# Kernel tuning notes

Measured on AMD Instinct MI355X. Metric: run time of the kernel, lower is better.

Reference implementation:

```python
import jax, jax.numpy as jnp
import numpy as np


def setup_inputs() -> dict:
    key = jax.random.key(0)
    kq, kk, kv = jax.random.split(key, 3)
    B, H, N, D = 4, 16, 2048, 64
    q = jax.random.normal(kq, (B, H, N, D), dtype=jnp.float32)
    k = jax.random.normal(kk, (B, N, D), dtype=jnp.float32)
    v = jax.random.normal(kv, (B, N, D), dtype=jnp.float32)
    return {"q": q, "k": k, "v": v}


def reference(q, k, v):
    # q: [B,H,N,D], k/v: [B,N,D] (KV shared across heads)
    scale = q.shape[-1] ** -0.5
    sim = jnp.einsum('bhid,bjd->bhij', q, k) * scale  # [B,H,N,N]
    attn = jax.nn.softmax(sim, axis=-1)
    return jnp.einsum('bhij,bjd->bhid', attn, v)  # [B,H,N,D]
```

## Files before the change

kernel.cpp:

```cpp
#include <hip/hip_runtime.h>
#include <hip/hip_bf16.h>

#define B_ 4
#define H_ 16
#define N_ 2048
#define D_ 64
#define BM 128

typedef __bf16 bf16;
typedef bf16 bf16x4 __attribute__((ext_vector_type(4)));
typedef bf16 bf16x8 __attribute__((ext_vector_type(8)));
typedef float f32x16 __attribute__((ext_vector_type(16)));
typedef unsigned u32x2 __attribute__((ext_vector_type(2)));
typedef unsigned u32x4 __attribute__((ext_vector_type(4)));

#define SCALE_LOG2E 0.18033688011112042f

#define GBL(p) ((const __attribute__((address_space(1))) void*)(p))
#define LDS(p) ((__attribute__((address_space(3))) void*)(p))

__global__ __launch_bounds__(512) void convert_kv(const float* __restrict__ k,
                                                  const float* __restrict__ v,
                                                  bf16* __restrict__ img) {
    __shared__ bf16 VT[64][66];
    const int tile = blockIdx.x;
    const int b = tile >> 5, T = tile & 31;
    const int t = threadIdx.x;
    bf16* timg = img + (size_t)tile * 8192;

    const int mtks = t >> 6;
    const int ln   = t & 63;
    const int mt = mtks >> 2, ks = mtks & 3;

    {
        const int kvr = T * 64 + mt * 32 + (ln & 31);
        const int d0  = ks * 16 + (ln >> 5) * 8;
        const float* src = k + ((size_t)b * N_ + kvr) * D_ + d0;
        float4 a = *(const float4*)src;
        float4 c = *(const float4*)(src + 4);
        bf16x8 o;
        o[0] = (bf16)a.x; o[1] = (bf16)a.y; o[2] = (bf16)a.z; o[3] = (bf16)a.w;
        o[4] = (bf16)c.x; o[5] = (bf16)c.y; o[6] = (bf16)c.z; o[7] = (bf16)c.w;
        *(bf16x8*)(timg + t * 8) = o;
    }

    {
        const int kv = t >> 3;
        const int c8 = (t & 7) * 8;
        const float* src = v + ((size_t)b * N_ + T * 64 + kv) * D_ + c8;
        float4 a = *(const float4*)src;
        float4 c = *(const float4*)(src + 4);
        VT[kv][c8 + 0] = (bf16)a.x; VT[kv][c8 + 1] = (bf16)a.y;
        VT[kv][c8 + 2] = (bf16)a.z; VT[kv][c8 + 3] = (bf16)a.w;
        VT[kv][c8 + 4] = (bf16)c.x; VT[kv][c8 + 5] = (bf16)c.y;
        VT[kv][c8 + 6] = (bf16)c.z; VT[kv][c8 + 7] = (bf16)c.w;
    }
    __syncthreads();
    {
        const int d   = mt * 32 + (ln & 31);
        const int kv0 = ks * 16 + (ln >> 5) * 8;
        bf16x8 o;
        #pragma unroll
        for (int j = 0; j < 8; ++j) o[j] = VT[kv0 + j][d];
        *(bf16x8*)(timg + 4096 + t * 8) = o;
    }
}

static __device__ inline bf16x4 pack4(float a, float b, float c, float d) {
    bf16x4 r; r[0] = (bf16)a; r[1] = (bf16)b; r[2] = (bf16)c; r[3] = (bf16)d; return r;
}

static __device__ inline bf16x8 cswap(bf16x4 lo, bf16x4 hi) {
    u32x2 l = __builtin_bit_cast(u32x2, lo);
    u32x2 h = __builtin_bit_cast(u32x2, hi);
    u32x2 r0 = __builtin_amdgcn_permlane32_swap(l[0], h[0], false, false);
    u32x2 r1 = __builtin_amdgcn_permlane32_swap(l[1], h[1], false, false);
    u32x4 o; o[0] = r0[0]; o[1] = r1[0]; o[2] = r0[1]; o[3] = r1[1];
    return __builtin_bit_cast(bf16x8, o);
}

__global__ __launch_bounds__(256, 2) void attn_fwd(const float* __restrict__ q,
                                                   const bf16* __restrict__ img,
                                                   float* __restrict__ out) {
    __shared__ __align__(16) bf16 KV3[3][8192];

    const int tid  = threadIdx.x;
    const int lane = tid & 63;
    const int wv   = tid >> 6;
    const int half = lane >> 5;
    const int l31  = lane & 31;

    const int bh = blockIdx.y;
    const int b  = bh >> 4;
    const int q0 = blockIdx.x * BM + wv * 32;

    const bf16* tiles = img + (size_t)b * 32 * 8192;

    bf16x8 qf[4];
    #pragma unroll
    for (int ks = 0; ks < 4; ++ks) {
        const float* src = q + ((size_t)bh * N_ + q0 + l31) * D_ + ks * 16 + half * 8;
        float4 a = *(const float4*)src;
        float4 c = *(const float4*)(src + 4);
        bf16x8 pk;
        pk[0] = (bf16)(a.x * SCALE_LOG2E); pk[1] = (bf16)(a.y * SCALE_LOG2E);
        pk[2] = (bf16)(a.z * SCALE_LOG2E); pk[3] = (bf16)(a.w * SCALE_LOG2E);
        pk[4] = (bf16)(c.x * SCALE_LOG2E); pk[5] = (bf16)(c.y * SCALE_LOG2E);
        pk[6] = (bf16)(c.z * SCALE_LOG2E); pk[7] = (bf16)(c.w * SCALE_LOG2E);
        qf[ks] = pk;
    }

    f32x16 acc[2] = {{}, {}};
    float lacc = 0.f;

    auto issue_dma = [&](int t, int sl) {
        const bf16* g = tiles + (size_t)t * 8192;
        #pragma unroll
        for (int j = 0; j < 4; ++j) {
            const int c = wv * 4 + j;
            __builtin_amdgcn_global_load_lds(GBL(g + c * 512 + lane * 8),
                                             LDS(&KV3[sl][c * 512]), 16, 0, 0);
        }
    };

    auto computeS = [&](int it, f32x16 (&s)[2]) {
        const bf16* bp = &KV3[it % 3][0];
        s[0] = f32x16{}; s[1] = f32x16{};
        #pragma unroll
        for (int ks = 0; ks < 4; ++ks) {
            bf16x8 k0 = *(const bf16x8*)&bp[((0 * 4 + ks) * 64 + lane) * 8];
            bf16x8 k1 = *(const bf16x8*)&bp[((1 * 4 + ks) * 64 + lane) * 8];
            s[0] = __builtin_amdgcn_mfma_f32_32x32x16_bf16(k0, qf[ks], s[0], 0, 0, 0);
            s[1] = __builtin_amdgcn_mfma_f32_32x32x16_bf16(k1, qf[ks], s[1], 0, 0, 0);
        }
    };
    auto softpv = [&](int it, const f32x16 (&s)[2]) {
        const bf16* vp = &KV3[it % 3][4096];
        #pragma unroll
        for (int mt = 0; mt < 2; ++mt) {
            #pragma unroll
            for (int sp = 0; sp < 2; ++sp) {
                const int g = mt * 2 + sp;
                bf16x8 v0 = *(const bf16x8*)&vp[((0 * 4 + g) * 64 + lane) * 8];
                bf16x8 v1 = *(const bf16x8*)&vp[((1 * 4 + g) * 64 + lane) * 8];
                float pv8[8];
                #pragma unroll
                for (int r = 0; r < 8; ++r) pv8[r] = __builtin_amdgcn_exp2f(s[mt][8 * sp + r]);
                lacc += ((pv8[0] + pv8[1]) + (pv8[2] + pv8[3]))
                      + ((pv8[4] + pv8[5]) + (pv8[6] + pv8[7]));
                bf16x4 lo = pack4(pv8[0], pv8[1], pv8[2], pv8[3]);
                bf16x4 hi = pack4(pv8[4], pv8[5], pv8[6], pv8[7]);
                bf16x8 bfrag = cswap(lo, hi);
                acc[0] = __builtin_amdgcn_mfma_f32_32x32x16_bf16(v0, bfrag, acc[0], 0, 0, 0);
                acc[1] = __builtin_amdgcn_mfma_f32_32x32x16_bf16(v1, bfrag, acc[1], 0, 0, 0);
            }
        }
    };

    f32x16 sA[2], sB[2];

    issue_dma(0, 0);
    __syncthreads();
    issue_dma(1, 1);
    computeS(0, sA);

    #pragma unroll 1
    for (int it = 1; it < 31; it += 2) {
        __syncthreads();
        issue_dma(it + 1, (it + 1) % 3);
        computeS(it, sB);
        softpv(it - 1, sA);
        __syncthreads();
        issue_dma(it + 2, (it + 2) % 3);
        computeS(it + 1, sA);
        softpv(it, sB);
    }
    __syncthreads();
    computeS(31, sB);
    softpv(30, sA);
    softpv(31, sB);

    float l = lacc + __shfl_xor(lacc, 32);
    float inv = 1.0f / l;
    const int qrow = q0 + l31;
    float* dst = out + ((size_t)bh * N_ + qrow) * D_ + 4 * half;
    #pragma unroll
    for (int mt = 0; mt < 2; ++mt)
        #pragma unroll
        for (int rq = 0; rq < 4; ++rq) {
            float4 o;
            o.x = acc[mt][4 * rq + 0] * inv;
            o.y = acc[mt][4 * rq + 1] * inv;
            o.z = acc[mt][4 * rq + 2] * inv;
            o.w = acc[mt][4 * rq + 3] * inv;
            *(float4*)(dst + mt * 32 + 8 * rq) = o;
        }
}

extern "C" void kernel_launch(void* const* d_in, const int* in_sizes, int n_in,
                              void* d_out, int out_size, void* d_ws, size_t ws_size,
                              hipStream_t stream) {
    const float* q = (const float*)d_in[0];
    const float* k = (const float*)d_in[1];
    const float* v = (const float*)d_in[2];
    float* out = (float*)d_out;

    bf16* img = (bf16*)d_ws;

    convert_kv<<<B_ * 32, 512, 0, stream>>>(k, v, img);
    dim3 grid(N_ / BM, B_ * H_);
    attn_fwd<<<grid, 256, 0, stream>>>(q, img, out);
}
```

Baseline: 152.5 us.

## Split S tiles into halves to cut registers and raise occupancy to three blocks

Result: slower. 156.8 us (+2.8%).

```diff
diff --git a/kernel.cpp b/kernel.cpp
--- a/kernel.cpp
+++ b/kernel.cpp
@@ -79,7 +79,7 @@
     return __builtin_bit_cast(bf16x8, o);
 }
 
-__global__ __launch_bounds__(256, 2) void attn_fwd(const float* __restrict__ q,
+__global__ __launch_bounds__(256, 3) void attn_fwd(const float* __restrict__ q,
                                                    const bf16* __restrict__ img,
                                                    float* __restrict__ out) {
     __shared__ __align__(16) bf16 KV3[3][8192];
@@ -123,62 +123,51 @@
         }
     };
 
-    auto computeS = [&](int it, f32x16 (&s)[2]) {
+    auto computeS_h = [&](int it, int mt, f32x16 &s) {
         const bf16* bp = &KV3[it % 3][0];
-        s[0] = f32x16{}; s[1] = f32x16{};
+        s = f32x16{};
         #pragma unroll
         for (int ks = 0; ks < 4; ++ks) {
-            bf16x8 k0 = *(const bf16x8*)&bp[((0 * 4 + ks) * 64 + lane) * 8];
-            bf16x8 k1 = *(const bf16x8*)&bp[((1 * 4 + ks) * 64 + lane) * 8];
-            s[0] = __builtin_amdgcn_mfma_f32_32x32x16_bf16(k0, qf[ks], s[0], 0, 0, 0);
-            s[1] = __builtin_amdgcn_mfma_f32_32x32x16_bf16(k1, qf[ks], s[1], 0, 0, 0);
+            bf16x8 kf = *(const bf16x8*)&bp[((mt * 4 + ks) * 64 + lane) * 8];
+            s = __builtin_amdgcn_mfma_f32_32x32x16_bf16(kf, qf[ks], s, 0, 0, 0);
         }
     };
-    auto softpv = [&](int it, const f32x16 (&s)[2]) {
+    auto softpv_h = [&](int it, int mt, const f32x16 &s) {
         const bf16* vp = &KV3[it % 3][4096];
         #pragma unroll
-        for (int mt = 0; mt < 2; ++mt) {
+        for (int sp = 0; sp < 2; ++sp) {
+            const int g = mt * 2 + sp;
+            bf16x8 v0 = *(const bf16x8*)&vp[((0 * 4 + g) * 64 + lane) * 8];
+            bf16x8 v1 = *(const bf16x8*)&vp[((1 * 4 + g) * 64 + lane) * 8];
+            float pv8[8];
             #pragma unroll
-            for (int sp = 0; sp < 2; ++sp) {
-                const int g = mt * 2 + sp;
-                bf16x8 v0 = *(const bf16x8*)&vp[((0 * 4 + g) * 64 + lane) * 8];
-                bf16x8 v1 = *(const bf16x8*)&vp[((1 * 4 + g) * 64 + lane) * 8];
-                float pv8[8];
-                #pragma unroll
-                for (int r = 0; r < 8; ++r) pv8[r] = __builtin_amdgcn_exp2f(s[mt][8 * sp + r]);
-                lacc += ((pv8[0] + pv8[1]) + (pv8[2] + pv8[3]))
-                      + ((pv8[4] + pv8[5]) + (pv8[6] + pv8[7]));
-                bf16x4 lo = pack4(pv8[0], pv8[1], pv8[2], pv8[3]);
-                bf16x4 hi = pack4(pv8[4], pv8[5], pv8[6], pv8[7]);
-                bf16x8 bfrag = cswap(lo, hi);
-                acc[0] = __builtin_amdgcn_mfma_f32_32x32x16_bf16(v0, bfrag, acc[0], 0, 0, 0);
-                acc[1] = __builtin_amdgcn_mfma_f32_32x32x16_bf16(v1, bfrag, acc[1], 0, 0, 0);
-            }
+            for (int r = 0; r < 8; ++r) pv8[r] = __builtin_amdgcn_exp2f(s[8 * sp + r]);
+            lacc += ((pv8[0] + pv8[1]) + (pv8[2] + pv8[3]))
+                  + ((pv8[4] + pv8[5]) + (pv8[6] + pv8[7]));
+            bf16x4 lo = pack4(pv8[0], pv8[1], pv8[2], pv8[3]);
+            bf16x4 hi = pack4(pv8[4], pv8[5], pv8[6], pv8[7]);
+            bf16x8 bfrag = cswap(lo, hi);
+            acc[0] = __builtin_amdgcn_mfma_f32_32x32x16_bf16(v0, bfrag, acc[0], 0, 0, 0);
+            acc[1] = __builtin_amdgcn_mfma_f32_32x32x16_bf16(v1, bfrag, acc[1], 0, 0, 0);
         }
     };
 
-    f32x16 sA[2], sB[2];
+    f32x16 sA, sB;
 
     issue_dma(0, 0);
     __syncthreads();
     issue_dma(1, 1);
-    computeS(0, sA);
+    computeS_h(0, 0, sA);
 
     #pragma unroll 1
-    for (int it = 1; it < 31; it += 2) {
+    for (int t = 0; t < 32; ++t) {
+        computeS_h(t, 1, sB);
+        softpv_h(t, 0, sA);
         __syncthreads();
-        issue_dma(it + 1, (it + 1) % 3);
-        computeS(it, sB);
-        softpv(it - 1, sA);
-        __syncthreads();
-        issue_dma(it + 2, (it + 2) % 3);
-        computeS(it + 1, sA);
-        softpv(it, sB);
-    }
-    __syncthreads();
-    computeS(31, sB);
-    softpv(30, sA);
-    softpv(31, sB);
+        if (t + 2 < 32) issue_dma(t + 2, (t + 2) % 3);
+        if (t + 1 < 32) computeS_h(t + 1, 0, sA);
+        softpv_h(t, 1, sB);
+    }
 
     float l = lacc + __shfl_xor(lacc, 32);
     float inv = 1.0f / l;
```

## Process two 32-row query sub-tiles per wave to reuse K/V fragments

Applied to the files above, without the earlier changes.

Result: slower. 157.1 us (+3.0%).

```diff
diff --git a/kernel.cpp b/kernel.cpp
--- a/kernel.cpp
+++ b/kernel.cpp
@@ -5,7 +5,7 @@
 #define H_ 16
 #define N_ 2048
 #define D_ 64
-#define BM 128
+#define BM 256
 
 typedef __bf16 bf16;
 typedef bf16 bf16x4 __attribute__((ext_vector_type(4)));
@@ -92,26 +92,28 @@
 
     const int bh = blockIdx.y;
     const int b  = bh >> 4;
-    const int q0 = blockIdx.x * BM + wv * 32;
+    const int q0 = blockIdx.x * BM + wv * 64;
 
     const bf16* tiles = img + (size_t)b * 32 * 8192;
 
-    bf16x8 qf[4];
+    bf16x8 qf[2][4];
     #pragma unroll
-    for (int ks = 0; ks < 4; ++ks) {
-        const float* src = q + ((size_t)bh * N_ + q0 + l31) * D_ + ks * 16 + half * 8;
-        float4 a = *(const float4*)src;
-        float4 c = *(const float4*)(src + 4);
-        bf16x8 pk;
-        pk[0] = (bf16)(a.x * SCALE_LOG2E); pk[1] = (bf16)(a.y * SCALE_LOG2E);
-        pk[2] = (bf16)(a.z * SCALE_LOG2E); pk[3] = (bf16)(a.w * SCALE_LOG2E);
-        pk[4] = (bf16)(c.x * SCALE_LOG2E); pk[5] = (bf16)(c.y * SCALE_LOG2E);
-        pk[6] = (bf16)(c.z * SCALE_LOG2E); pk[7] = (bf16)(c.w * SCALE_LOG2E);
-        qf[ks] = pk;
-    }
-
-    f32x16 acc[2] = {{}, {}};
-    float lacc = 0.f;
+    for (int qn = 0; qn < 2; ++qn)
+        #pragma unroll
+        for (int ks = 0; ks < 4; ++ks) {
+            const float* src = q + ((size_t)bh * N_ + q0 + qn * 32 + l31) * D_ + ks * 16 + half * 8;
+            float4 a = *(const float4*)src;
+            float4 c = *(const float4*)(src + 4);
+            bf16x8 pk;
+            pk[0] = (bf16)(a.x * SCALE_LOG2E); pk[1] = (bf16)(a.y * SCALE_LOG2E);
+            pk[2] = (bf16)(a.z * SCALE_LOG2E); pk[3] = (bf16)(a.w * SCALE_LOG2E);
+            pk[4] = (bf16)(c.x * SCALE_LOG2E); pk[5] = (bf16)(c.y * SCALE_LOG2E);
+            pk[6] = (bf16)(c.z * SCALE_LOG2E); pk[7] = (bf16)(c.w * SCALE_LOG2E);
+            qf[qn][ks] = pk;
+        }
+
+    f32x16 acc[2][2] = {{{}, {}}, {{}, {}}};
+    float lacc[2] = {0.f, 0.f};
 
     auto issue_dma = [&](int t, int sl) {
         const bf16* g = tiles + (size_t)t * 8192;
@@ -123,18 +125,18 @@
         }
     };
 
-    auto computeS = [&](int it, f32x16 (&s)[2]) {
+    auto computeS = [&](int it, int qn, f32x16 (&s)[2]) {
         const bf16* bp = &KV3[it % 3][0];
         s[0] = f32x16{}; s[1] = f32x16{};
         #pragma unroll
         for (int ks = 0; ks < 4; ++ks) {
             bf16x8 k0 = *(const bf16x8*)&bp[((0 * 4 + ks) * 64 + lane) * 8];
             bf16x8 k1 = *(const bf16x8*)&bp[((1 * 4 + ks) * 64 + lane) * 8];
-            s[0] = __builtin_amdgcn_mfma_f32_32x32x16_bf16(k0, qf[ks], s[0], 0, 0, 0);
-            s[1] = __builtin_amdgcn_mfma_f32_32x32x16_bf16(k1, qf[ks], s[1], 0, 0, 0);
+            s[0] = __builtin_amdgcn_mfma_f32_32x32x16_bf16(k0, qf[qn][ks], s[0], 0, 0, 0);
+            s[1] = __builtin_amdgcn_mfma_f32_32x32x16_bf16(k1, qf[qn][ks], s[1], 0, 0, 0);
         }
     };
-    auto softpv = [&](int it, const f32x16 (&s)[2]) {
+    auto softpv = [&](int it, int qn, const f32x16 (&s)[2]) {
         const bf16* vp = &KV3[it % 3][4096];
         #pragma unroll
         for (int mt = 0; mt < 2; ++mt) {
@@ -146,55 +148,55 @@
                 float pv8[8];
                 #pragma unroll
                 for (int r = 0; r < 8; ++r) pv8[r] = __builtin_amdgcn_exp2f(s[mt][8 * sp + r]);
-                lacc += ((pv8[0] + pv8[1]) + (pv8[2] + pv8[3]))
-                      + ((pv8[4] + pv8[5]) + (pv8[6] + pv8[7]));
+                lacc[qn] += ((pv8[0] + pv8[1]) + (pv8[2] + pv8[3]))
+                          + ((pv8[4] + pv8[5]) + (pv8[6] + pv8[7]));
                 bf16x4 lo = pack4(pv8[0], pv8[1], pv8[2], pv8[3]);
                 bf16x4 hi = pack4(pv8[4], pv8[5], pv8[6], pv8[7]);
                 bf16x8 bfrag = cswap(lo, hi);
-                acc[0] = __builtin_amdgcn_mfma_f32_32x32x16_bf16(v0, bfrag, acc[0], 0, 0, 0);
-                acc[1] = __builtin_amdgcn_mfma_f32_32x32x16_bf16(v1, bfrag, acc[1], 0, 0, 0);
+                acc[0][qn] = __builtin_amdgcn_mfma_f32_32x32x16_bf16(v0, bfrag, acc[0][qn], 0, 0, 0);
+                acc[1][qn] = __builtin_amdgcn_mfma_f32_32x32x16_bf16(v1, bfrag, acc[1][qn], 0, 0, 0);
             }
         }
     };
 
-    f32x16 sA[2], sB[2];
+    f32x16 sQ0[2], sQ1[2];
 
     issue_dma(0, 0);
     __syncthreads();
     issue_dma(1, 1);
-    computeS(0, sA);
+    computeS(0, 0, sQ0);
+    computeS(0, 1, sQ1);
 
     #pragma unroll 1
-    for (int it = 1; it < 31; it += 2) {
+    for (int t = 0; t < 31; ++t) {
         __syncthreads();
-        issue_dma(it + 1, (it + 1) % 3);
-        computeS(it, sB);
-        softpv(it - 1, sA);
-        __syncthreads();
-        issue_dma(it + 2, (it + 2) % 3);
-        computeS(it + 1, sA);
-        softpv(it, sB);
-    }
-    __syncthreads();
-    computeS(31, sB);
-    softpv(30, sA);
-    softpv(31, sB);
-
-    float l = lacc + __shfl_xor(lacc, 32);
-    float inv = 1.0f / l;
-    const int qrow = q0 + l31;
-    float* dst = out + ((size_t)bh * N_ + qrow) * D_ + 4 * half;
+        if (t + 2 < 32) issue_dma(t + 2, (t + 2) % 3);
+        softpv(t, 0, sQ0);
+        computeS(t + 1, 0, sQ0);
+        softpv(t, 1, sQ1);
+        computeS(t + 1, 1, sQ1);
+    }
+    softpv(31, 0, sQ0);
+    softpv(31, 1, sQ1);
+
     #pragma unroll
-    for (int mt = 0; mt < 2; ++mt)
-        #pragma unroll
-        for (int rq = 0; rq < 4; ++rq) {
-            float4 o;
-            o.x = acc[mt][4 * rq + 0] * inv;
-            o.y = acc[mt][4 * rq + 1] * inv;
-            o.z = acc[mt][4 * rq + 2] * inv;
-            o.w = acc[mt][4 * rq + 3] * inv;
-            *(float4*)(dst + mt * 32 + 8 * rq) = o;
-        }
+    for (int qn = 0; qn < 2; ++qn) {
+        float l = lacc[qn] + __shfl_xor(lacc[qn], 32);
+        float inv = 1.0f / l;
+        const int qrow = q0 + qn * 32 + l31;
+        float* dst = out + ((size_t)bh * N_ + qrow) * D_ + 4 * half;
+        #pragma unroll
+        for (int mt = 0; mt < 2; ++mt)
+            #pragma unroll
+            for (int rq = 0; rq < 4; ++rq) {
+                float4 o;
+                o.x = acc[mt][qn][4 * rq + 0] * inv;
+                o.y = acc[mt][qn][4 * rq + 1] * inv;
+                o.z = acc[mt][qn][4 * rq + 2] * inv;
+                o.w = acc[mt][qn][4 * rq + 3] * inv;
+                *(float4*)(dst + mt * 32 + 8 * rq) = o;
+            }
+    }
 }
 
 extern "C" void kernel_launch(void* const* d_in, const int* in_sizes, int n_in,
```
